# Performance work log

Hardware: AMD Instinct MI355X
Metric: run time of the kernel (lower is better)

The kernel has to match this reference:

```python
import jax, jax.numpy as jnp
import numpy as np

N_NODES = 100000
K = 10
ALPHA = 0.1


def _gcn_norm(ei, n):
    # add self loops (PyG APPNP default: add_self_loops=True, gcn_norm)
    loops = jnp.arange(n, dtype=ei.dtype)
    src = jnp.concatenate([ei[0], loops])
    dst = jnp.concatenate([ei[1], loops])
    ones = jnp.ones(src.shape[0], dtype=jnp.float32)
    deg = jax.ops.segment_sum(ones, dst, num_segments=n)
    dinv = jnp.where(deg > 0, jax.lax.rsqrt(deg), 0.0)
    norm = dinv[src] * dinv[dst]  # [E+N]
    return src, dst, norm


def reference(x, ei, W1, b1, W2, b2):
    n = x.shape[0]
    # MLP encoder (dropout is identity in eval mode)
    h = jax.nn.relu(x @ W1 + b1)
    h = h @ W2 + b2  # [N, out_c]
    src, dst, norm = _gcn_norm(ei, n)
    h0 = h
    for _ in range(K):
        msg = norm[:, None] * h[src]                      # gather [E+N, out_c]
        agg = jax.ops.segment_sum(msg, dst, num_segments=n)  # scatter-add
        h = (1.0 - ALPHA) * agg + ALPHA * h0
    return h


def setup_inputs() -> dict:
    key = jax.random.key(0)
    k1, k2, k3, k4 = jax.random.split(key, 4)
    in_c, hidden, out_c = 512, 256, 64
    E = 3200000
    x = jax.random.normal(k1, (N_NODES, in_c), dtype=jnp.float32)
    ei = jax.random.randint(k2, (2, E), 0, N_NODES, dtype=jnp.int64)
    s1 = 1.0 / np.sqrt(in_c)
    s2 = 1.0 / np.sqrt(hidden)
    W1 = jax.random.uniform(k3, (in_c, hidden), jnp.float32, -s1, s1)
    b1 = jnp.zeros((hidden,), jnp.float32)
    W2 = jax.random.uniform(k4, (hidden, out_c), jnp.float32, -s2, s2)
    b2 = jnp.zeros((out_c,), jnp.float32)
    return {"x": x, "ei": ei, "W1": W1, "b1": b1, "W2": W2, "b2": b2}
```

## Files before the change

### kernel.cpp

```cpp
#include <hip/hip_runtime.h>


typedef unsigned short u16;
typedef unsigned int   u32;
typedef __bf16    bfx8  __attribute__((ext_vector_type(8)));
typedef _Float16  h16x8 __attribute__((ext_vector_type(8)));
typedef float     f32x4 __attribute__((ext_vector_type(4)));

#define CAP 4096
#define EPB 16384
#define NBMAX 1792

__device__ __forceinline__ u16 f2bf(float f) {
    u32 u = __float_as_uint(f);
    u += 0x7fffu + ((u >> 16) & 1u);
    return (u16)(u >> 16);
}


__global__ __launch_bounds__(256) void binscat_kernel(
        const int* __restrict__ src, const int* __restrict__ dst,
        int* __restrict__ gcur, u32* __restrict__ binned, int E, int NB) {
    __shared__ int cnt[NBMAX];
    int tid = threadIdx.x;
#pragma unroll
    for (int j = 0; j < NBMAX / 256; ++j) cnt[tid + j * 256] = 0;
    __syncthreads();
    int e0 = blockIdx.x * EPB;
    for (int r = 0; r < EPB / 256; ++r) {
        int i = e0 + r * 256 + tid;
        if (i < E) atomicAdd(&cnt[dst[i] >> 6], 1);
    }
    __syncthreads();
    for (int j = 0; j < NBMAX / 256; ++j) {
        int b = tid + j * 256;
        if (b < NB) {
            int c = cnt[b];
            cnt[b] = (c > 0) ? atomicAdd(&gcur[b], c) : 0;
        }
    }
    __syncthreads();
    for (int r = 0; r < EPB / 256; ++r) {
        int i = e0 + r * 256 + tid;
        if (i < E) {
            int d = dst[i];
            int s = src[i];
            int bb = d >> 6;
            int p = atomicAdd(&cnt[bb], 1);
            if (p < CAP) binned[(size_t)bb * CAP + p] = ((u32)(d & 63) << 17) | (u32)s;
        }
    }
}


__global__ __launch_bounds__(256) void bucket_scan_kernel(
        const int* __restrict__ gcur, int* __restrict__ bbase,
        int* __restrict__ rp, int N, int NB) {
    __shared__ int tsum[256];
    int tid = threadIdx.x;
    int loc[7];
    int run = 0;
#pragma unroll
    for (int j = 0; j < 7; ++j) {
        int b = tid * 7 + j;
        int v = 0;
        if (b < NB) { v = gcur[b]; if (v > CAP) v = CAP; }
        loc[j] = run;
        run += v;
    }
    tsum[tid] = run;
    __syncthreads();
    for (int off = 1; off < 256; off <<= 1) {
        int t = (tid >= off) ? tsum[tid - off] : 0;
        __syncthreads();
        tsum[tid] += t;
        __syncthreads();
    }
    int texcl = tsum[tid] - run;
#pragma unroll
    for (int j = 0; j < 7; ++j) {
        int b = tid * 7 + j;
        if (b < NB) bbase[b] = texcl + loc[j];
    }
    if (tid == 255) rp[N] = tsum[255];
}


__global__ __launch_bounds__(256) void buildcsr_kernel(
        const u32* __restrict__ binned, const int* __restrict__ gcur,
        const int* __restrict__ bbase, int* __restrict__ rp,
        float* __restrict__ dinv, int* __restrict__ csr, int N) {
    __shared__ u32 eb[CAP];
    __shared__ int lcsr[CAP];
    __shared__ int ncnt[64];
    __shared__ int lcur[64];
    int b = blockIdx.x;
    int tid = threadIdx.x;
    int cnt = gcur[b]; if (cnt > CAP) cnt = CAP;
    int base = bbase[b];
    if (tid < 64) ncnt[tid] = 0;
    __syncthreads();
    for (int idx = tid; idx < cnt; idx += 256) {
        u32 v = binned[(size_t)b * CAP + idx];
        eb[idx] = v;
        atomicAdd(&ncnt[v >> 17], 1);
    }
    __syncthreads();
    if (tid < 64) {
        int c = ncnt[tid];
        int s = c;
#pragma unroll
        for (int off = 1; off < 64; off <<= 1) {
            int t = __shfl_up(s, off);
            if (tid >= off) s += t;
        }
        int excl = s - c;
        lcur[tid] = excl;
        int node = b * 64 + tid;
        if (node < N) {
            rp[node] = base + excl;
            dinv[node] = rsqrtf(1.0f + (float)c);
        }
    }
    __syncthreads();
    for (int idx = tid; idx < cnt; idx += 256) {
        u32 v = eb[idx];
        int p = atomicAdd(&lcur[v >> 17], 1);
        lcsr[p] = (int)(v & 0x1FFFFu);
    }
    __syncthreads();
    for (int idx = tid; idx < cnt; idx += 256)
        csr[base + idx] = lcsr[idx];
}


__global__ void prepw1_kernel(const float* __restrict__ W1, u16* __restrict__ W1f) {
    int f = blockIdx.x * 256 + threadIdx.x;
    int lane = f & 63;
    int nt = (f >> 6) & 3;
    int w  = (f >> 8) & 3;
    int t  = f >> 10;
    int col = w * 64 + nt * 16 + (lane & 15);
    int k0  = t * 32 + ((lane >> 4) << 3);
    u32 pk[4];
#pragma unroll
    for (int j = 0; j < 4; ++j) {
        u16 lo = f2bf(W1[(size_t)(k0 + 2 * j) * 256 + col]);
        u16 hi = f2bf(W1[(size_t)(k0 + 2 * j + 1) * 256 + col]);
        pk[j] = (u32)lo | ((u32)hi << 16);
    }
    *(uint4*)&W1f[(size_t)f * 8] = make_uint4(pk[0], pk[1], pk[2], pk[3]);
}

__global__ void prepw2_kernel(const float* __restrict__ W2, u16* __restrict__ W2f) {
    int f = blockIdx.x * 256 + threadIdx.x;
    int lane = f & 63;
    int nt = (f >> 6) & 3;
    int t  = f >> 8;
    int col = nt * 16 + (lane & 15);
    int k0  = t * 32 + ((lane >> 4) << 3);
    u32 pk[4];
#pragma unroll
    for (int j = 0; j < 4; ++j) {
        u16 lo = f2bf(W2[(size_t)(k0 + 2 * j) * 64 + col]);
        u16 hi = f2bf(W2[(size_t)(k0 + 2 * j + 1) * 64 + col]);
        pk[j] = (u32)lo | ((u32)hi << 16);
    }
    *(uint4*)&W2f[(size_t)f * 8] = make_uint4(pk[0], pk[1], pk[2], pk[3]);
}


__global__ __launch_bounds__(256) void mlp_kernel(
        const float* __restrict__ x, const u16* __restrict__ W1f,
        const float* __restrict__ b1, const u16* __restrict__ W2f,
        const float* __restrict__ b2, const float* __restrict__ dinv,
        float* __restrict__ h0, _Float16* __restrict__ hA, int N) {
    __shared__ char lds[32768];
    u16* xs  = (u16*)lds;
    u16* h1s = (u16*)lds;

    const int tid  = threadIdx.x;
    const int wave = tid >> 6;
    const int lane = tid & 63;
    const int lq   = lane >> 4;
    const int lr   = lane & 15;
    const int blockRow = blockIdx.x * 64;

    const int sr = tid >> 2;
    const int sc = (tid & 3) << 3;
    const int gr = blockRow + sr;
    const bool haveRow = (gr < N);
    const float* xp = x + (size_t)(haveRow ? gr : 0) * 512 + sc;

    f32x4 acc[4][4];
#pragma unroll
    for (int a = 0; a < 4; ++a)
#pragma unroll
        for (int b = 0; b < 4; ++b) acc[a][b] = (f32x4){0.f, 0.f, 0.f, 0.f};

    {
        float v[8];
#pragma unroll
        for (int j = 0; j < 8; ++j) v[j] = 0.f;
        if (haveRow) {
            float4 u0 = *(const float4*)(xp);
            float4 u1 = *(const float4*)(xp + 4);
            v[0]=u0.x; v[1]=u0.y; v[2]=u0.z; v[3]=u0.w;
            v[4]=u1.x; v[5]=u1.y; v[6]=u1.z; v[7]=u1.w;
        }
        u32 pk[4];
#pragma unroll
        for (int j = 0; j < 4; ++j)
            pk[j] = (u32)f2bf(v[2*j]) | ((u32)f2bf(v[2*j+1]) << 16);
        *(uint4*)&xs[sr * 40 + sc] = make_uint4(pk[0], pk[1], pk[2], pk[3]);
    }

    const bfx8* w1q = (const bfx8*)W1f;

    for (int t = 0; t < 16; ++t) {
        bfx8 fb0 = w1q[(t * 16 + wave * 4 + 0) * 64 + lane];
        bfx8 fb1 = w1q[(t * 16 + wave * 4 + 1) * 64 + lane];
        bfx8 fb2 = w1q[(t * 16 + wave * 4 + 2) * 64 + lane];
        bfx8 fb3 = w1q[(t * 16 + wave * 4 + 3) * 64 + lane];
        float v[8];
#pragma unroll
        for (int j = 0; j < 8; ++j) v[j] = 0.f;
        if (t < 15 && haveRow) {
            const float* p = xp + (t + 1) * 32;
            float4 u0 = *(const float4*)(p);
            float4 u1 = *(const float4*)(p + 4);
            v[0]=u0.x; v[1]=u0.y; v[2]=u0.z; v[3]=u0.w;
            v[4]=u1.x; v[5]=u1.y; v[6]=u1.z; v[7]=u1.w;
        }
        __syncthreads();
        const u16* cur = xs + (t & 1) * 2560;
        bfx8 fa[4];
#pragma unroll
        for (int mt = 0; mt < 4; ++mt)
            fa[mt] = *(const bfx8*)&cur[(mt * 16 + lr) * 40 + lq * 8];
#pragma unroll
        for (int mt = 0; mt < 4; ++mt) {
            acc[mt][0] = __builtin_amdgcn_mfma_f32_16x16x32_bf16(fa[mt], fb0, acc[mt][0], 0, 0, 0);
            acc[mt][1] = __builtin_amdgcn_mfma_f32_16x16x32_bf16(fa[mt], fb1, acc[mt][1], 0, 0, 0);
            acc[mt][2] = __builtin_amdgcn_mfma_f32_16x16x32_bf16(fa[mt], fb2, acc[mt][2], 0, 0, 0);
            acc[mt][3] = __builtin_amdgcn_mfma_f32_16x16x32_bf16(fa[mt], fb3, acc[mt][3], 0, 0, 0);
        }
        if (t < 15) {
            u16* nxt = xs + ((t + 1) & 1) * 2560;
            u32 pk[4];
#pragma unroll
            for (int j = 0; j < 4; ++j)
                pk[j] = (u32)f2bf(v[2*j]) | ((u32)f2bf(v[2*j+1]) << 16);
            *(uint4*)&nxt[sr * 40 + sc] = make_uint4(pk[0], pk[1], pk[2], pk[3]);
        }
    }
    __syncthreads();

#pragma unroll
    for (int nt = 0; nt < 4; ++nt) {
        int col = wave * 64 + nt * 16 + lr;
        float bb = b1[col];
#pragma unroll
        for (int mt = 0; mt < 4; ++mt)
#pragma unroll
            for (int r = 0; r < 4; ++r) {
                int row = mt * 16 + lq * 4 + r;
                float vv = acc[mt][nt][r] + bb;
                vv = vv > 0.f ? vv : 0.f;
                h1s[row * 256 + (col ^ ((row & 7) << 3))] = f2bf(vv);
            }
    }
    __syncthreads();

    f32x4 acc2[4];
#pragma unroll
    for (int a = 0; a < 4; ++a) acc2[a] = (f32x4){0.f, 0.f, 0.f, 0.f};
    const bfx8* w2q = (const bfx8*)W2f;
    const int row2 = wave * 16 + lr;
    const int sw2  = (row2 & 7) << 3;
#pragma unroll
    for (int t2 = 0; t2 < 8; ++t2) {
        bfx8 a = *(const bfx8*)&h1s[row2 * 256 + ((t2 * 32 + lq * 8) ^ sw2)];
#pragma unroll
        for (int nt = 0; nt < 4; ++nt) {
            bfx8 b = w2q[(t2 * 4 + nt) * 64 + lane];
            acc2[nt] = __builtin_amdgcn_mfma_f32_16x16x32_bf16(a, b, acc2[nt], 0, 0, 0);
        }
    }

#pragma unroll
    for (int nt = 0; nt < 4; ++nt) {
        int col = nt * 16 + lr;
        float bb = b2[col];
#pragma unroll
        for (int r = 0; r < 4; ++r) {
            int row = wave * 16 + lq * 4 + r;
            int g = blockRow + row;
            if (g < N) {
                float vv = acc2[nt][r] + bb;
                size_t idx = (size_t)g * 64 + col;
                h0[idx] = vv;
                hA[idx] = (_Float16)(vv * dinv[g]);
            }
        }
    }
}


template <typename OUTT>
__global__ __launch_bounds__(256) void prop_kernel(
        const _Float16* __restrict__ hs, const float* __restrict__ h0,
        const float* __restrict__ dinv, const int* __restrict__ rp,
        const int* __restrict__ csr, OUTT* __restrict__ hout, int N) {
    int t = blockIdx.x * 256 + threadIdx.x;
    int i = t >> 3;
    int l = t & 7;
    if (i >= N) return;
    int beg = rp[i], end = rp[i + 1];
    const _Float16* hb = hs + l * 8;
    h16x8 self = *(const h16x8*)(hb + (size_t)i * 64);
    float a[8];
#pragma unroll
    for (int j = 0; j < 8; ++j) a[j] = (float)self[j];
    int e = beg;
    for (; e + 1 < end; e += 2) {
        int s0 = csr[e], s1 = csr[e + 1];
        h16x8 g0 = *(const h16x8*)(hb + (size_t)s0 * 64);
        h16x8 g1 = *(const h16x8*)(hb + (size_t)s1 * 64);
#pragma unroll
        for (int j = 0; j < 8; ++j) a[j] += (float)g0[j];
#pragma unroll
        for (int j = 0; j < 8; ++j) a[j] += (float)g1[j];
    }
    if (e < end) {
        int s0 = csr[e];
        h16x8 g0 = *(const h16x8*)(hb + (size_t)s0 * 64);
#pragma unroll
        for (int j = 0; j < 8; ++j) a[j] += (float)g0[j];
    }
    float dv = dinv[i];
    float c1 = 0.9f * dv;
    const float* h0p = h0 + (size_t)i * 64 + l * 8;
    float o[8];
#pragma unroll
    for (int j = 0; j < 8; ++j) o[j] = fmaf(c1, a[j], 0.1f * h0p[j]);
    if constexpr (sizeof(OUTT) == 2) {
        h16x8 ov;
#pragma unroll
        for (int j = 0; j < 8; ++j) ov[j] = (_Float16)(dv * o[j]);
        *(h16x8*)(hout + (size_t)i * 64 + l * 8) = ov;
    } else {
        float4* q = (float4*)(hout + (size_t)i * 64 + l * 8);
        q[0] = make_float4(o[0], o[1], o[2], o[3]);
        q[1] = make_float4(o[4], o[5], o[6], o[7]);
    }
}


extern "C" void kernel_launch(void* const* d_in, const int* in_sizes, int n_in,
                              void* d_out, int out_size, void* d_ws, size_t ws_size,
                              hipStream_t stream) {
    const float* x  = (const float*)d_in[0];
    const int*   ei = (const int*)d_in[1];
    const float* W1 = (const float*)d_in[2];
    const float* b1 = (const float*)d_in[3];
    const float* W2 = (const float*)d_in[4];
    const float* b2 = (const float*)d_in[5];
    const int N = in_sizes[0] / 512;
    const int E = in_sizes[1] / 2;
    const int NB = (N + 63) / 64;
    const int* src = ei;
    const int* dst = ei + E;

    char* w = (char*)d_ws;
    size_t off = 0;
    auto alloc = [&](size_t bytes) -> char* {
        char* p = w + off;
        off = (off + bytes + 1023) & ~(size_t)1023;
        return p;
    };
    int*      gcur  = (int*)alloc((size_t)NB * 4);
    int*      bbase = (int*)alloc((size_t)NB * 4);
    int*      rp    = (int*)alloc(((size_t)N + 1) * 4);
    float*    dinv  = (float*)alloc((size_t)N * 4);
    int*      csr   = (int*)alloc((size_t)E * 4);
    u32*      binned= (u32*)alloc((size_t)NB * CAP * 4);
    u16*      W1f   = (u16*)alloc(512 * 256 * 2);
    u16*      W2f   = (u16*)alloc(256 * 64 * 2);
    float*    h0    = (float*)alloc((size_t)N * 64 * 4);
    _Float16* hA    = (_Float16*)alloc((size_t)N * 64 * 2);
    _Float16* hB    = (_Float16*)alloc((size_t)N * 64 * 2);

    hipMemsetAsync(gcur, 0, (size_t)NB * 4, stream);
    binscat_kernel<<<(E + EPB - 1) / EPB, 256, 0, stream>>>(src, dst, gcur, binned, E, NB);
    bucket_scan_kernel<<<1, 256, 0, stream>>>(gcur, bbase, rp, N, NB);
    buildcsr_kernel<<<NB, 256, 0, stream>>>(binned, gcur, bbase, rp, dinv, csr, N);
    prepw1_kernel<<<64, 256, 0, stream>>>(W1, W1f);
    prepw2_kernel<<<8, 256, 0, stream>>>(W2, W2f);
    mlp_kernel<<<(N + 63) / 64, 256, 0, stream>>>(x, W1f, b1, W2f, b2, dinv, h0, hA, N);

    const _Float16* pin = hA;
    int grid = (N * 8 + 255) / 256;
    for (int it = 0; it < 9; ++it) {
        _Float16* pout = (it & 1) ? hA : hB;
        prop_kernel<_Float16><<<grid, 256, 0, stream>>>(pin, h0, dinv, rp, csr, pout, N);
        pin = pout;
    }
    prop_kernel<float><<<grid, 256, 0, stream>>>(pin, h0, dinv, rp, csr, (float*)d_out, N);
}
```

Baseline: 1.056 ms.

## Split propagation features into four column slices and load MLP inputs directly

The fp16 propagation buffers are relaid out as four 16-column slabs, and propagation launches a 2D grid with one slab per y-block. Each node's gathered rows then fall inside a slab of 3.2 MB, which should fit in cache and improve gather hit rates, at the cost of four passes over the CSR indices and 4-byte gathers per lane. Separately, the MLP kernel drops its LDS double-buffered staging of x and builds bf16 MFMA fragments straight from global float4 loads. This removes the barriers but makes the x reads less coalesced.

```diff
diff --git a/kernel.cpp b/kernel.cpp
--- a/kernel.cpp
+++ b/kernel.cpp
@@ -5,6 +5,7 @@
 typedef unsigned int   u32;
 typedef __bf16    bfx8  __attribute__((ext_vector_type(8)));
 typedef _Float16  h16x8 __attribute__((ext_vector_type(8)));
+typedef _Float16  h16x2 __attribute__((ext_vector_type(2)));
 typedef float     f32x4 __attribute__((ext_vector_type(4)));
 
 #define CAP 4096
@@ -15,6 +16,15 @@
     u32 u = __float_as_uint(f);
     u += 0x7fffu + ((u >> 16) & 1u);
     return (u16)(u >> 16);
+}
+
+__device__ __forceinline__ bfx8 pack_bf8(float4 a, float4 b) {
+    union { u32 u[4]; bfx8 v; } c;
+    c.u[0] = (u32)f2bf(a.x) | ((u32)f2bf(a.y) << 16);
+    c.u[1] = (u32)f2bf(a.z) | ((u32)f2bf(a.w) << 16);
+    c.u[2] = (u32)f2bf(b.x) | ((u32)f2bf(b.y) << 16);
+    c.u[3] = (u32)f2bf(b.z) | ((u32)f2bf(b.w) << 16);
+    return c.v;
 }
 
 
@@ -175,9 +185,7 @@
         const float* __restrict__ b1, const u16* __restrict__ W2f,
         const float* __restrict__ b2, const float* __restrict__ dinv,
         float* __restrict__ h0, _Float16* __restrict__ hA, int N) {
-    __shared__ char lds[32768];
-    u16* xs  = (u16*)lds;
-    u16* h1s = (u16*)lds;
+    __shared__ u16 h1s[64 * 256];
 
     const int tid  = threadIdx.x;
     const int wave = tid >> 6;
@@ -186,11 +194,14 @@
     const int lr   = lane & 15;
     const int blockRow = blockIdx.x * 64;
 
-    const int sr = tid >> 2;
-    const int sc = (tid & 3) << 3;
-    const int gr = blockRow + sr;
-    const bool haveRow = (gr < N);
-    const float* xp = x + (size_t)(haveRow ? gr : 0) * 512 + sc;
+    const float* xr[4];
+    bool vr[4];
+#pragma unroll
+    for (int mt = 0; mt < 4; ++mt) {
+        int r = blockRow + mt * 16 + lr;
+        vr[mt] = (r < N);
+        xr[mt] = x + (size_t)(vr[mt] ? r : 0) * 512 + lq * 8;
+    }
 
     f32x4 acc[4][4];
 #pragma unroll
@@ -198,63 +209,30 @@
 #pragma unroll
         for (int b = 0; b < 4; ++b) acc[a][b] = (f32x4){0.f, 0.f, 0.f, 0.f};
 
-    {
-        float v[8];
-#pragma unroll
-        for (int j = 0; j < 8; ++j) v[j] = 0.f;
-        if (haveRow) {
-            float4 u0 = *(const float4*)(xp);
-            float4 u1 = *(const float4*)(xp + 4);
-            v[0]=u0.x; v[1]=u0.y; v[2]=u0.z; v[3]=u0.w;
-            v[4]=u1.x; v[5]=u1.y; v[6]=u1.z; v[7]=u1.w;
-        }
-        u32 pk[4];
-#pragma unroll
-        for (int j = 0; j < 4; ++j)
-            pk[j] = (u32)f2bf(v[2*j]) | ((u32)f2bf(v[2*j+1]) << 16);
-        *(uint4*)&xs[sr * 40 + sc] = make_uint4(pk[0], pk[1], pk[2], pk[3]);
-    }
-
     const bfx8* w1q = (const bfx8*)W1f;
-
+    const float4 z4 = make_float4(0.f, 0.f, 0.f, 0.f);
+
+#pragma unroll 2
     for (int t = 0; t < 16; ++t) {
-        bfx8 fb0 = w1q[(t * 16 + wave * 4 + 0) * 64 + lane];
-        bfx8 fb1 = w1q[(t * 16 + wave * 4 + 1) * 64 + lane];
-        bfx8 fb2 = w1q[(t * 16 + wave * 4 + 2) * 64 + lane];
-        bfx8 fb3 = w1q[(t * 16 + wave * 4 + 3) * 64 + lane];
-        float v[8];
-#pragma unroll
-        for (int j = 0; j < 8; ++j) v[j] = 0.f;
-        if (t < 15 && haveRow) {
-            const float* p = xp + (t + 1) * 32;
-            float4 u0 = *(const float4*)(p);
-            float4 u1 = *(const float4*)(p + 4);
-            v[0]=u0.x; v[1]=u0.y; v[2]=u0.z; v[3]=u0.w;
-            v[4]=u1.x; v[5]=u1.y; v[6]=u1.z; v[7]=u1.w;
-        }
-        __syncthreads();
-        const u16* cur = xs + (t & 1) * 2560;
+        bfx8 fb[4];
+#pragma unroll
+        for (int n = 0; n < 4; ++n)
+            fb[n] = w1q[(t * 16 + wave * 4 + n) * 64 + lane];
         bfx8 fa[4];
 #pragma unroll
-        for (int mt = 0; mt < 4; ++mt)
-            fa[mt] = *(const bfx8*)&cur[(mt * 16 + lr) * 40 + lq * 8];
-#pragma unroll
         for (int mt = 0; mt < 4; ++mt) {
-            acc[mt][0] = __builtin_amdgcn_mfma_f32_16x16x32_bf16(fa[mt], fb0, acc[mt][0], 0, 0, 0);
-            acc[mt][1] = __builtin_amdgcn_mfma_f32_16x16x32_bf16(fa[mt], fb1, acc[mt][1], 0, 0, 0);
-            acc[mt][2] = __builtin_amdgcn_mfma_f32_16x16x32_bf16(fa[mt], fb2, acc[mt][2], 0, 0, 0);
-            acc[mt][3] = __builtin_amdgcn_mfma_f32_16x16x32_bf16(fa[mt], fb3, acc[mt][3], 0, 0, 0);
-        }
-        if (t < 15) {
-            u16* nxt = xs + ((t + 1) & 1) * 2560;
-            u32 pk[4];
-#pragma unroll
-            for (int j = 0; j < 4; ++j)
-                pk[j] = (u32)f2bf(v[2*j]) | ((u32)f2bf(v[2*j+1]) << 16);
-            *(uint4*)&nxt[sr * 40 + sc] = make_uint4(pk[0], pk[1], pk[2], pk[3]);
-        }
-    }
-    __syncthreads();
+            float4 u0 = vr[mt] ? *(const float4*)(xr[mt] + t * 32)     : z4;
+            float4 u1 = vr[mt] ? *(const float4*)(xr[mt] + t * 32 + 4) : z4;
+            fa[mt] = pack_bf8(u0, u1);
+        }
+#pragma unroll
+        for (int mt = 0; mt < 4; ++mt) {
+            acc[mt][0] = __builtin_amdgcn_mfma_f32_16x16x32_bf16(fa[mt], fb[0], acc[mt][0], 0, 0, 0);
+            acc[mt][1] = __builtin_amdgcn_mfma_f32_16x16x32_bf16(fa[mt], fb[1], acc[mt][1], 0, 0, 0);
+            acc[mt][2] = __builtin_amdgcn_mfma_f32_16x16x32_bf16(fa[mt], fb[2], acc[mt][2], 0, 0, 0);
+            acc[mt][3] = __builtin_amdgcn_mfma_f32_16x16x32_bf16(fa[mt], fb[3], acc[mt][3], 0, 0, 0);
+        }
+    }
 
 #pragma unroll
     for (int nt = 0; nt < 4; ++nt) {
@@ -298,9 +276,8 @@
             int g = blockRow + row;
             if (g < N) {
                 float vv = acc2[nt][r] + bb;
-                size_t idx = (size_t)g * 64 + col;
-                h0[idx] = vv;
-                hA[idx] = (_Float16)(vv * dinv[g]);
+                h0[(size_t)g * 64 + col] = vv;
+                hA[(size_t)nt * N * 16 + (size_t)g * 16 + lr] = (_Float16)(vv * dinv[g]);
             }
         }
     }
@@ -312,47 +289,45 @@
         const _Float16* __restrict__ hs, const float* __restrict__ h0,
         const float* __restrict__ dinv, const int* __restrict__ rp,
         const int* __restrict__ csr, OUTT* __restrict__ hout, int N) {
+    const int s = blockIdx.y;
     int t = blockIdx.x * 256 + threadIdx.x;
     int i = t >> 3;
     int l = t & 7;
     if (i >= N) return;
     int beg = rp[i], end = rp[i + 1];
-    const _Float16* hb = hs + l * 8;
-    h16x8 self = *(const h16x8*)(hb + (size_t)i * 64);
-    float a[8];
-#pragma unroll
-    for (int j = 0; j < 8; ++j) a[j] = (float)self[j];
+    const _Float16* hb = hs + (size_t)s * N * 16 + l * 2;
+    h16x2 self = *(const h16x2*)(hb + (size_t)i * 16);
+    float a0 = (float)self[0];
+    float a1 = (float)self[1];
     int e = beg;
-    for (; e + 1 < end; e += 2) {
-        int s0 = csr[e], s1 = csr[e + 1];
-        h16x8 g0 = *(const h16x8*)(hb + (size_t)s0 * 64);
-        h16x8 g1 = *(const h16x8*)(hb + (size_t)s1 * 64);
-#pragma unroll
-        for (int j = 0; j < 8; ++j) a[j] += (float)g0[j];
-#pragma unroll
-        for (int j = 0; j < 8; ++j) a[j] += (float)g1[j];
-    }
-    if (e < end) {
+    for (; e + 3 < end; e += 4) {
+        int s0 = csr[e], s1 = csr[e + 1], s2 = csr[e + 2], s3 = csr[e + 3];
+        h16x2 g0 = *(const h16x2*)(hb + (size_t)s0 * 16);
+        h16x2 g1 = *(const h16x2*)(hb + (size_t)s1 * 16);
+        h16x2 g2 = *(const h16x2*)(hb + (size_t)s2 * 16);
+        h16x2 g3 = *(const h16x2*)(hb + (size_t)s3 * 16);
+        a0 += (float)g0[0]; a1 += (float)g0[1];
+        a0 += (float)g1[0]; a1 += (float)g1[1];
+        a0 += (float)g2[0]; a1 += (float)g2[1];
+        a0 += (float)g3[0]; a1 += (float)g3[1];
+    }
+    for (; e < end; ++e) {
         int s0 = csr[e];
-        h16x8 g0 = *(const h16x8*)(hb + (size_t)s0 * 64);
-#pragma unroll
-        for (int j = 0; j < 8; ++j) a[j] += (float)g0[j];
+        h16x2 g0 = *(const h16x2*)(hb + (size_t)s0 * 16);
+        a0 += (float)g0[0]; a1 += (float)g0[1];
     }
     float dv = dinv[i];
     float c1 = 0.9f * dv;
-    const float* h0p = h0 + (size_t)i * 64 + l * 8;
-    float o[8];
-#pragma unroll
-    for (int j = 0; j < 8; ++j) o[j] = fmaf(c1, a[j], 0.1f * h0p[j]);
+    const float* h0p = h0 + (size_t)i * 64 + s * 16 + l * 2;
+    float o0 = fmaf(c1, a0, 0.1f * h0p[0]);
+    float o1 = fmaf(c1, a1, 0.1f * h0p[1]);
     if constexpr (sizeof(OUTT) == 2) {
-        h16x8 ov;
-#pragma unroll
-        for (int j = 0; j < 8; ++j) ov[j] = (_Float16)(dv * o[j]);
-        *(h16x8*)(hout + (size_t)i * 64 + l * 8) = ov;
+        h16x2 ov;
+        ov[0] = (_Float16)(dv * o0);
+        ov[1] = (_Float16)(dv * o1);
+        *(h16x2*)((_Float16*)hout + (size_t)s * N * 16 + (size_t)i * 16 + l * 2) = ov;
     } else {
-        float4* q = (float4*)(hout + (size_t)i * 64 + l * 8);
-        q[0] = make_float4(o[0], o[1], o[2], o[3]);
-        q[1] = make_float4(o[4], o[5], o[6], o[7]);
+        *(float2*)((float*)hout + (size_t)i * 64 + s * 16 + l * 2) = make_float2(o0, o1);
     }
 }
 
@@ -400,11 +375,11 @@
     mlp_kernel<<<(N + 63) / 64, 256, 0, stream>>>(x, W1f, b1, W2f, b2, dinv, h0, hA, N);
 
     const _Float16* pin = hA;
-    int grid = (N * 8 + 255) / 256;
+    dim3 pgrid((N * 8 + 255) / 256, 4);
     for (int it = 0; it < 9; ++it) {
         _Float16* pout = (it & 1) ? hA : hB;
-        prop_kernel<_Float16><<<grid, 256, 0, stream>>>(pin, h0, dinv, rp, csr, pout, N);
+        prop_kernel<_Float16><<<pgrid, 256, 0, stream>>>(pin, h0, dinv, rp, csr, pout, N);
         pin = pout;
     }
-    prop_kernel<float><<<grid, 256, 0, stream>>>(pin, h0, dinv, rp, csr, (float*)d_out, N);
-}
+    prop_kernel<float><<<pgrid, 256, 0, stream>>>(pin, h0, dinv, rp, csr, (float*)d_out, N);
+}
```

Result: slower. 1.786 ms (+69.0%).

## Sub-sort CSR by source range and interleave four nodes per lane group in propagation

Applied to the files above, without the earlier changes.

The CSR build now sorts each node's neighbours into 32 source-range sub-buckets and records per-sub-bucket counts in a 16-bit table. Each propagation thread group handles four nodes and walks their sub-buckets in lockstep, so gathers from all warps move through the source feature array range by range. The aim is better L2 locality for the random gathers. The cost is an extra count table read per node, more LDS work and a block-wide scan in the CSR build, more registers, and serialised per-node inner loops that can diverge within a wave.

```diff
diff --git a/kernel.cpp b/kernel.cpp
--- a/kernel.cpp
+++ b/kernel.cpp
@@ -89,47 +89,67 @@
 __global__ __launch_bounds__(256) void buildcsr_kernel(
         const u32* __restrict__ binned, const int* __restrict__ gcur,
         const int* __restrict__ bbase, int* __restrict__ rp,
-        float* __restrict__ dinv, int* __restrict__ csr, int N) {
+        u16* __restrict__ cnt16, float* __restrict__ dinv,
+        int* __restrict__ csr, int N) {
     __shared__ u32 eb[CAP];
     __shared__ int lcsr[CAP];
-    __shared__ int ncnt[64];
-    __shared__ int lcur[64];
+    __shared__ int cnt2[2048];
+    __shared__ int cur2[2048];
+    __shared__ int tsum[256];
     int b = blockIdx.x;
     int tid = threadIdx.x;
-    int cnt = gcur[b]; if (cnt > CAP) cnt = CAP;
+    int cntB = gcur[b]; if (cntB > CAP) cntB = CAP;
     int base = bbase[b];
-    if (tid < 64) ncnt[tid] = 0;
-    __syncthreads();
-    for (int idx = tid; idx < cnt; idx += 256) {
+#pragma unroll
+    for (int j = 0; j < 8; ++j) cnt2[tid * 8 + j] = 0;
+    __syncthreads();
+    for (int idx = tid; idx < cntB; idx += 256) {
         u32 v = binned[(size_t)b * CAP + idx];
         eb[idx] = v;
-        atomicAdd(&ncnt[v >> 17], 1);
+        int key = (int)(((v >> 17) << 5) | ((v & 0x1FFFFu) >> 12));
+        atomicAdd(&cnt2[key], 1);
+    }
+    __syncthreads();
+    int loc[8];
+    int run = 0;
+#pragma unroll
+    for (int j = 0; j < 8; ++j) { loc[j] = run; run += cnt2[tid * 8 + j]; }
+    tsum[tid] = run;
+    __syncthreads();
+    for (int off = 1; off < 256; off <<= 1) {
+        int t = (tid >= off) ? tsum[tid - off] : 0;
+        __syncthreads();
+        tsum[tid] += t;
+        __syncthreads();
+    }
+    int texcl = tsum[tid] - run;
+#pragma unroll
+    for (int j = 0; j < 8; ++j) cur2[tid * 8 + j] = texcl + loc[j];
+    {
+        u16 pk[8];
+#pragma unroll
+        for (int j = 0; j < 8; ++j) pk[j] = (u16)cnt2[tid * 8 + j];
+        *(uint4*)&cnt16[(size_t)b * 2048 + tid * 8] = *(uint4*)pk;
     }
     __syncthreads();
     if (tid < 64) {
-        int c = ncnt[tid];
-        int s = c;
-#pragma unroll
-        for (int off = 1; off < 64; off <<= 1) {
-            int t = __shfl_up(s, off);
-            if (tid >= off) s += t;
-        }
-        int excl = s - c;
-        lcur[tid] = excl;
         int node = b * 64 + tid;
+        int lo = cur2[tid * 32];
+        int hi = (tid == 63) ? cntB : cur2[(tid + 1) * 32];
         if (node < N) {
-            rp[node] = base + excl;
-            dinv[node] = rsqrtf(1.0f + (float)c);
-        }
-    }
-    __syncthreads();
-    for (int idx = tid; idx < cnt; idx += 256) {
+            rp[node] = base + lo;
+            dinv[node] = rsqrtf(1.0f + (float)(hi - lo));
+        }
+    }
+    __syncthreads();
+    for (int idx = tid; idx < cntB; idx += 256) {
         u32 v = eb[idx];
-        int p = atomicAdd(&lcur[v >> 17], 1);
+        int key = (int)(((v >> 17) << 5) | ((v & 0x1FFFFu) >> 12));
+        int p = atomicAdd(&cur2[key], 1);
         lcsr[p] = (int)(v & 0x1FFFFu);
     }
     __syncthreads();
-    for (int idx = tid; idx < cnt; idx += 256)
+    for (int idx = tid; idx < cntB; idx += 256)
         csr[base + idx] = lcsr[idx];
 }
 
@@ -287,7 +307,6 @@
             acc2[nt] = __builtin_amdgcn_mfma_f32_16x16x32_bf16(a, b, acc2[nt], 0, 0, 0);
         }
     }
-
 #pragma unroll
     for (int nt = 0; nt < 4; ++nt) {
         int col = nt * 16 + lr;
@@ -311,48 +330,75 @@
 __global__ __launch_bounds__(256) void prop_kernel(
         const _Float16* __restrict__ hs, const float* __restrict__ h0,
         const float* __restrict__ dinv, const int* __restrict__ rp,
-        const int* __restrict__ csr, OUTT* __restrict__ hout, int N) {
-    int t = blockIdx.x * 256 + threadIdx.x;
-    int i = t >> 3;
-    int l = t & 7;
-    if (i >= N) return;
-    int beg = rp[i], end = rp[i + 1];
-    const _Float16* hb = hs + l * 8;
-    h16x8 self = *(const h16x8*)(hb + (size_t)i * 64);
-    float a[8];
-#pragma unroll
-    for (int j = 0; j < 8; ++j) a[j] = (float)self[j];
-    int e = beg;
-    for (; e + 1 < end; e += 2) {
-        int s0 = csr[e], s1 = csr[e + 1];
-        h16x8 g0 = *(const h16x8*)(hb + (size_t)s0 * 64);
-        h16x8 g1 = *(const h16x8*)(hb + (size_t)s1 * 64);
-#pragma unroll
-        for (int j = 0; j < 8; ++j) a[j] += (float)g0[j];
-#pragma unroll
-        for (int j = 0; j < 8; ++j) a[j] += (float)g1[j];
-    }
-    if (e < end) {
-        int s0 = csr[e];
-        h16x8 g0 = *(const h16x8*)(hb + (size_t)s0 * 64);
-#pragma unroll
-        for (int j = 0; j < 8; ++j) a[j] += (float)g0[j];
-    }
-    float dv = dinv[i];
-    float c1 = 0.9f * dv;
-    const float* h0p = h0 + (size_t)i * 64 + l * 8;
-    float o[8];
-#pragma unroll
-    for (int j = 0; j < 8; ++j) o[j] = fmaf(c1, a[j], 0.1f * h0p[j]);
-    if constexpr (sizeof(OUTT) == 2) {
-        h16x8 ov;
-#pragma unroll
-        for (int j = 0; j < 8; ++j) ov[j] = (_Float16)(dv * o[j]);
-        *(h16x8*)(hout + (size_t)i * 64 + l * 8) = ov;
-    } else {
-        float4* q = (float4*)(hout + (size_t)i * 64 + l * 8);
-        q[0] = make_float4(o[0], o[1], o[2], o[3]);
-        q[1] = make_float4(o[4], o[5], o[6], o[7]);
+        const u16* __restrict__ cnt16, const int* __restrict__ csr,
+        OUTT* __restrict__ hout, int N) {
+    const int tid  = threadIdx.x;
+    const int wid  = (blockIdx.x << 2) + (tid >> 6);
+    const int lane = tid & 63;
+    const int sl   = lane >> 3;
+    const int l    = lane & 7;
+    const int nbase = wid * 32 + sl;
+
+    float a[4][8];
+    int e[4];
+    int nodes[4];
+    bool val[4];
+#pragma unroll
+    for (int g = 0; g < 4; ++g) {
+        int i = nbase + g * 8;
+        nodes[g] = i;
+        val[g] = (i < N);
+        int ii = val[g] ? i : 0;
+        e[g] = rp[ii];
+        h16x8 self = *(const h16x8*)(hs + (size_t)ii * 64 + l * 8);
+#pragma unroll
+        for (int j = 0; j < 8; ++j) a[g][j] = (float)self[j];
+    }
+
+    for (int rb = 0; rb < 4; ++rb) {
+        uint4 cv[4];
+#pragma unroll
+        for (int g = 0; g < 4; ++g)
+            cv[g] = *(const uint4*)&cnt16[(size_t)(val[g] ? nodes[g] : 0) * 32 + rb * 8];
+#pragma unroll
+        for (int rr = 0; rr < 8; ++rr) {
+#pragma unroll
+            for (int g = 0; g < 4; ++g) {
+                u32 w = ((const u32*)&cv[g])[rr >> 1];
+                int c = (int)((w >> ((rr & 1) << 4)) & 0xFFFFu);
+                if (!val[g]) c = 0;
+                int ee = e[g];
+                e[g] = ee + c;
+                for (int k = 0; k < c; ++k) {
+                    int s0 = csr[ee + k];
+                    h16x8 gv = *(const h16x8*)(hs + (size_t)s0 * 64 + l * 8);
+#pragma unroll
+                    for (int j = 0; j < 8; ++j) a[g][j] += (float)gv[j];
+                }
+            }
+        }
+    }
+
+#pragma unroll
+    for (int g = 0; g < 4; ++g) {
+        if (!val[g]) continue;
+        int i = nodes[g];
+        float dv = dinv[i];
+        float c1 = 0.9f * dv;
+        const float* h0p = h0 + (size_t)i * 64 + l * 8;
+        float o[8];
+#pragma unroll
+        for (int j = 0; j < 8; ++j) o[j] = fmaf(c1, a[g][j], 0.1f * h0p[j]);
+        if constexpr (sizeof(OUTT) == 2) {
+            h16x8 ov;
+#pragma unroll
+            for (int j = 0; j < 8; ++j) ov[j] = (_Float16)(dv * o[j]);
+            *(h16x8*)((_Float16*)hout + (size_t)i * 64 + l * 8) = ov;
+        } else {
+            float* op = (float*)hout + (size_t)i * 64 + l * 8;
+            *(float4*)op       = make_float4(o[0], o[1], o[2], o[3]);
+            *(float4*)(op + 4) = make_float4(o[4], o[5], o[6], o[7]);
+        }
     }
 }
 
@@ -383,6 +429,7 @@
     int*      bbase = (int*)alloc((size_t)NB * 4);
     int*      rp    = (int*)alloc(((size_t)N + 1) * 4);
     float*    dinv  = (float*)alloc((size_t)N * 4);
+    u16*      cnt16 = (u16*)alloc((size_t)NB * 2048 * 2);
     int*      csr   = (int*)alloc((size_t)E * 4);
     u32*      binned= (u32*)alloc((size_t)NB * CAP * 4);
     u16*      W1f   = (u16*)alloc(512 * 256 * 2);
@@ -394,17 +441,17 @@
     hipMemsetAsync(gcur, 0, (size_t)NB * 4, stream);
     binscat_kernel<<<(E + EPB - 1) / EPB, 256, 0, stream>>>(src, dst, gcur, binned, E, NB);
     bucket_scan_kernel<<<1, 256, 0, stream>>>(gcur, bbase, rp, N, NB);
-    buildcsr_kernel<<<NB, 256, 0, stream>>>(binned, gcur, bbase, rp, dinv, csr, N);
+    buildcsr_kernel<<<NB, 256, 0, stream>>>(binned, gcur, bbase, rp, cnt16, dinv, csr, N);
     prepw1_kernel<<<64, 256, 0, stream>>>(W1, W1f);
     prepw2_kernel<<<8, 256, 0, stream>>>(W2, W2f);
     mlp_kernel<<<(N + 63) / 64, 256, 0, stream>>>(x, W1f, b1, W2f, b2, dinv, h0, hA, N);
 
     const _Float16* pin = hA;
-    int grid = (N * 8 + 255) / 256;
+    int pgrid = (N + 127) / 128;
     for (int it = 0; it < 9; ++it) {
         _Float16* pout = (it & 1) ? hA : hB;
-        prop_kernel<_Float16><<<grid, 256, 0, stream>>>(pin, h0, dinv, rp, csr, pout, N);
+        prop_kernel<_Float16><<<pgrid, 256, 0, stream>>>(pin, h0, dinv, rp, cnt16, csr, pout, N);
         pin = pout;
     }
-    prop_kernel<float><<<grid, 256, 0, stream>>>(pin, h0, dinv, rp, csr, (float*)d_out, N);
-}
+    prop_kernel<float><<<pgrid, 256, 0, stream>>>(pin, h0, dinv, rp, cnt16, csr, (float*)d_out, N);
+}
```

New measurement: 2.457 ms. 133% more time.

## Sub-sort CSR neighbors by source chunk and unroll gather loop by four

Applied to the files above, without the earlier changes.

The CSR build now buckets each destination's edges by a coarse source-index chunk (src>>12), using a 2048-entry shared histogram and a block-wide scan. Each node's neighbor list therefore comes out roughly sorted by source, which should improve locality for the gathers in the propagation kernel. The propagation loop is also unrolled from 2 to 4 neighbors, putting more independent loads in flight per thread. The cost is a heavier build kernel (larger shared arrays, a multi-step scan with many syncs) and more registers in the propagation kernel.

```diff
diff --git a/kernel.cpp b/kernel.cpp
--- a/kernel.cpp
+++ b/kernel.cpp
@@ -92,44 +92,57 @@
         float* __restrict__ dinv, int* __restrict__ csr, int N) {
     __shared__ u32 eb[CAP];
     __shared__ int lcsr[CAP];
-    __shared__ int ncnt[64];
-    __shared__ int lcur[64];
+    __shared__ int cnt2[2048];
+    __shared__ int cur2[2048];
+    __shared__ int tsum[256];
     int b = blockIdx.x;
     int tid = threadIdx.x;
-    int cnt = gcur[b]; if (cnt > CAP) cnt = CAP;
+    int cntB = gcur[b]; if (cntB > CAP) cntB = CAP;
     int base = bbase[b];
-    if (tid < 64) ncnt[tid] = 0;
-    __syncthreads();
-    for (int idx = tid; idx < cnt; idx += 256) {
+#pragma unroll
+    for (int j = 0; j < 8; ++j) cnt2[tid * 8 + j] = 0;
+    __syncthreads();
+    for (int idx = tid; idx < cntB; idx += 256) {
         u32 v = binned[(size_t)b * CAP + idx];
         eb[idx] = v;
-        atomicAdd(&ncnt[v >> 17], 1);
-    }
+        int key = (int)(((v >> 17) << 5) | ((v & 0x1FFFFu) >> 12));
+        atomicAdd(&cnt2[key], 1);
+    }
+    __syncthreads();
+    int loc[8];
+    int run = 0;
+#pragma unroll
+    for (int j = 0; j < 8; ++j) { loc[j] = run; run += cnt2[tid * 8 + j]; }
+    tsum[tid] = run;
+    __syncthreads();
+    for (int off = 1; off < 256; off <<= 1) {
+        int t = (tid >= off) ? tsum[tid - off] : 0;
+        __syncthreads();
+        tsum[tid] += t;
+        __syncthreads();
+    }
+    int texcl = tsum[tid] - run;
+#pragma unroll
+    for (int j = 0; j < 8; ++j) cur2[tid * 8 + j] = texcl + loc[j];
     __syncthreads();
     if (tid < 64) {
-        int c = ncnt[tid];
-        int s = c;
-#pragma unroll
-        for (int off = 1; off < 64; off <<= 1) {
-            int t = __shfl_up(s, off);
-            if (tid >= off) s += t;
-        }
-        int excl = s - c;
-        lcur[tid] = excl;
         int node = b * 64 + tid;
+        int lo = cur2[tid * 32];
+        int hi = (tid == 63) ? cntB : cur2[(tid + 1) * 32];
         if (node < N) {
-            rp[node] = base + excl;
-            dinv[node] = rsqrtf(1.0f + (float)c);
-        }
-    }
-    __syncthreads();
-    for (int idx = tid; idx < cnt; idx += 256) {
+            rp[node] = base + lo;
+            dinv[node] = rsqrtf(1.0f + (float)(hi - lo));
+        }
+    }
+    __syncthreads();
+    for (int idx = tid; idx < cntB; idx += 256) {
         u32 v = eb[idx];
-        int p = atomicAdd(&lcur[v >> 17], 1);
+        int key = (int)(((v >> 17) << 5) | ((v & 0x1FFFFu) >> 12));
+        int p = atomicAdd(&cur2[key], 1);
         lcsr[p] = (int)(v & 0x1FFFFu);
     }
     __syncthreads();
-    for (int idx = tid; idx < cnt; idx += 256)
+    for (int idx = tid; idx < cntB; idx += 256)
         csr[base + idx] = lcsr[idx];
 }
 
@@ -287,7 +300,6 @@
             acc2[nt] = __builtin_amdgcn_mfma_f32_16x16x32_bf16(a, b, acc2[nt], 0, 0, 0);
         }
     }
-
 #pragma unroll
     for (int nt = 0; nt < 4; ++nt) {
         int col = nt * 16 + lr;
@@ -323,16 +335,22 @@
 #pragma unroll
     for (int j = 0; j < 8; ++j) a[j] = (float)self[j];
     int e = beg;
-    for (; e + 1 < end; e += 2) {
-        int s0 = csr[e], s1 = csr[e + 1];
+    for (; e + 3 < end; e += 4) {
+        int s0 = csr[e], s1 = csr[e + 1], s2 = csr[e + 2], s3 = csr[e + 3];
         h16x8 g0 = *(const h16x8*)(hb + (size_t)s0 * 64);
         h16x8 g1 = *(const h16x8*)(hb + (size_t)s1 * 64);
+        h16x8 g2 = *(const h16x8*)(hb + (size_t)s2 * 64);
+        h16x8 g3 = *(const h16x8*)(hb + (size_t)s3 * 64);
 #pragma unroll
         for (int j = 0; j < 8; ++j) a[j] += (float)g0[j];
 #pragma unroll
         for (int j = 0; j < 8; ++j) a[j] += (float)g1[j];
-    }
-    if (e < end) {
+#pragma unroll
+        for (int j = 0; j < 8; ++j) a[j] += (float)g2[j];
+#pragma unroll
+        for (int j = 0; j < 8; ++j) a[j] += (float)g3[j];
+    }
+    for (; e < end; ++e) {
         int s0 = csr[e];
         h16x8 g0 = *(const h16x8*)(hb + (size_t)s0 * 64);
 #pragma unroll
```

Measured after the change: 981.6 us. 1.08x faster.
